# Performance work log

Measured on AMD Instinct MI355X. Metric: run time of the kernel, lower is better.

The kernel has to match this reference:

```python
import jax, jax.numpy as jnp
import numpy as np

B = 512      # batch = envs * nagents
M = 32       # nmodels
NAG = 8      # nagents
H = 256      # hidsz
NACT = 16    # nactions


def _lm(x, W, b, ids):
    # LinearMulti: per-example weight selected by model id.
    # x: [B, I], W: [M, I, O], b: [M, O], ids: [B] -> [B, O]
    return jnp.einsum('bi,bio->bo', x, W[ids]) + b[ids]


def setup_inputs() -> dict:
    key = jax.random.key(0)
    ks = jax.random.split(key, 16)
    s = 0.02
    return {
        'comm_in': jax.random.normal(ks[0], (B, NAG, H), jnp.float32),
        'inp': jnp.zeros((B, 1), jnp.int32),  # Embedding table has 1 row -> only index 0 valid
        'prev_hid': jax.random.normal(ks[1], (B, H), jnp.float32),
        'prev_cell': jnp.zeros((B, H), jnp.float32),  # unused in rnn branch, kept for signature fidelity
        'model_ids': jax.random.randint(ks[2], (B,), 0, M),
        # comm2hid LinearMulti (comm_encoder): hidsz -> hidsz
        'Wc': jax.random.normal(ks[3], (M, H, H), jnp.float32) * s,
        'bc': jax.random.normal(ks[4], (M, H), jnp.float32) * s,
        # rnn LinearMulti: hidsz -> hidsz
        'Wr': jax.random.normal(ks[5], (M, H, H), jnp.float32) * s,
        'br': jax.random.normal(ks[6], (M, H), jnp.float32) * s,
        # action LinearMulti: hidsz -> nactions
        'Wa': jax.random.normal(ks[7], (M, H, NACT), jnp.float32) * s,
        'ba': jax.random.normal(ks[8], (M, NACT), jnp.float32) * s,
        # baseline LinearMulti: hidsz -> 1
        'Wb': jax.random.normal(ks[9], (M, H, 1), jnp.float32) * s,
        'bb': jax.random.normal(ks[10], (M, 1), jnp.float32) * s,
        # comm_out LinearMulti (fully_connected): hidsz -> hidsz * nagents
        'Wo': jax.random.normal(ks[11], (M, H, H * NAG), jnp.float32) * s,
        'bo': jax.random.normal(ks[12], (M, H * NAG), jnp.float32) * s,
        # Encoder: Embedding(1, hidsz) + bias
        'lut': jax.random.normal(ks[13], (1, H), jnp.float32) * s,
        'enc_bias': jax.random.normal(ks[14], (H,), jnp.float32) * s,
    }


def reference(comm_in, inp, prev_hid, prev_cell, model_ids,
              Wc, bc, Wr, br, Wa, ba, Wb, bb, Wo, bo, lut, enc_bias):
    # __comm2hid: sum agent messages, then model-id-routed linear
    comm2hid = _lm(jnp.sum(comm_in, axis=1), Wc, bc, model_ids)  # [B, H]
    # Encoder: embedding lookup, sum over token dim, add bias
    enc = jnp.sum(lut[inp], axis=1) + enc_bias                   # [B, H]
    # _rnn: sum of encoder, routed recurrent linear, and comm; tanh gate
    hidstate = jnp.tanh(enc + _lm(prev_hid, Wr, br, model_ids) + comm2hid)
    # __action
    action_prob = jax.nn.softmax(_lm(hidstate, Wa, ba, model_ids), axis=-1)  # [B, NACT]
    baseline = _lm(hidstate, Wb, bb, model_ids)                              # [B, 1]
    # __comm_out (fully_connected): routed linear then divide by nagents-1
    comm_out = _lm(hidstate, Wo, bo, model_ids) / (NAG - 1)                  # [B, H*NAG]
    return (action_prob, baseline, hidstate, comm_out)
```

## Files before the change

kernel.cpp:

```cpp
#include <hip/hip_runtime.h>


constexpr int Bn = 512, Mn = 32, NAGn = 8, Hn = 256, NACTn = 16;
constexpr int On = Hn * NAGn;
constexpr int En = 32;
constexpr int EW = 8;

__device__ __forceinline__ void gl_lds16(const float* g, float* l) {
  __builtin_amdgcn_global_load_lds(
      (const __attribute__((address_space(1))) void*)g,
      (__attribute__((address_space(3))) void*)l, 16, 0, 0);
}


__global__ __launch_bounds__(512) void k_group(const int* __restrict__ ids,
                                               int* __restrict__ list32) {
  __shared__ int scnt[Mn];
  int t = threadIdx.x;
  if (t < Mn) scnt[t] = 0;
  list32[t] = -1;
  list32[t + 512] = -1;
  __syncthreads();
  int m = ids[t];
  int pos = atomicAdd(&scnt[m], 1);
  if (pos < En) list32[m * En + pos] = t;
}

__global__ __launch_bounds__(256) void k_pack(
    const float* __restrict__ comm_in, const float* __restrict__ prev_hid,
    const int* __restrict__ list32, float* __restrict__ xcat) {
  int m = blockIdx.x, half = blockIdx.y;
  int tid = threadIdx.x;
  __shared__ float buf[En][Hn + 1];
  __shared__ int lst[En];
  if (tid < En) lst[tid] = list32[m * En + tid];
  __syncthreads();
  if (half == 0) {
    for (int j = 0; j < En; j++) {
      int e = lst[j];
      float s = 0.f;
      if (e >= 0) {
        const float* cp = comm_in + (size_t)e * NAGn * Hn + tid;
#pragma unroll
        for (int a = 0; a < NAGn; a++) s += cp[a * Hn];
      }
      buf[j][tid] = s;
    }
  } else {
    for (int j = 0; j < En; j++) {
      int e = lst[j];
      buf[j][tid] = (e >= 0) ? prev_hid[e * Hn + tid] : 0.f;
    }
  }
  __syncthreads();
  int j = tid & 31, kr = tid >> 5;
  float* xm = xcat + ((size_t)m * 512 + half * Hn) * En;
  for (int k0 = 0; k0 < Hn; k0 += 8) {
    int k = k0 + kr;
    xm[(size_t)k * En + j] = buf[j][k];
  }
}

__global__ __launch_bounds__(256) void k_lin(
    const float* __restrict__ Wc, const float* __restrict__ Wr,
    const float* __restrict__ xcat, const int* __restrict__ list32,
    float* __restrict__ acc_hid) {
  int ct = blockIdx.x, kc = blockIdx.y, m = blockIdx.z;
  if (list32[m * En] < 0) return;
  int tid = threadIdx.x, w = tid >> 6, lane = tid & 63;
  __shared__ alignas(16) float xbuf[128 * En];
  __shared__ alignas(16) float wbuf[2][32 * 128];

  const float* W = (kc < 2) ? (Wc + ((size_t)m * Hn + kc * 128) * Hn)
                            : (Wr + ((size_t)m * Hn + (kc - 2) * 128) * Hn);
  const float* wsrc = W + ct * 128;
  const float* xsrc = xcat + ((size_t)m * 512 + kc * 128) * En;
#pragma unroll
  for (int q = 0; q < 4; q++) {
    int c = w * 4 + q;
    gl_lds16(xsrc + c * 256 + lane * 4, xbuf + c * 256);
  }
#pragma unroll
  for (int q = 0; q < 4; q++) {
    int c = w * 4 + q;
    int row = c * 2 + (lane >> 5);
    gl_lds16(wsrc + (size_t)row * Hn + (lane & 31) * 4, wbuf[0] + c * 256);
  }
  bool act = list32[m * En + w * EW] >= 0;
  float2 acc[EW];
#pragma unroll
  for (int j = 0; j < EW; j++) acc[j] = make_float2(0.f, 0.f);
  __syncthreads();

  for (int t = 0; t < 4; t++) {
    if (t < 3) {
      const float* ws2 = wsrc + (size_t)(t + 1) * 32 * Hn;
#pragma unroll
      for (int q = 0; q < 4; q++) {
        int c = w * 4 + q;
        int row = c * 2 + (lane >> 5);
        gl_lds16(ws2 + (size_t)row * Hn + (lane & 31) * 4, wbuf[(t + 1) & 1] + c * 256);
      }
    }
    if (act) {
      const float* wb = wbuf[t & 1] + lane * 2;
      const float* xb = xbuf + (size_t)(t * 32) * En + w * EW;
#pragma unroll 8
      for (int k = 0; k < 32; k++) {
        float2 wv = *(const float2*)(wb + k * 128);
        float4 xa = *(const float4*)(xb + k * En);
        float4 xc = *(const float4*)(xb + k * En + 4);
        acc[0].x += xa.x * wv.x; acc[0].y += xa.x * wv.y;
        acc[1].x += xa.y * wv.x; acc[1].y += xa.y * wv.y;
        acc[2].x += xa.z * wv.x; acc[2].y += xa.z * wv.y;
        acc[3].x += xa.w * wv.x; acc[3].y += xa.w * wv.y;
        acc[4].x += xc.x * wv.x; acc[4].y += xc.x * wv.y;
        acc[5].x += xc.y * wv.x; acc[5].y += xc.y * wv.y;
        acc[6].x += xc.z * wv.x; acc[6].y += xc.z * wv.y;
        acc[7].x += xc.w * wv.x; acc[7].y += xc.w * wv.y;
      }
    }
    __syncthreads();
  }
  if (act) {
    float* ap = acc_hid + ((size_t)m * En + w * EW) * Hn + ct * 128 + lane * 2;
#pragma unroll
    for (int j = 0; j < EW; j++) {
      atomicAdd(ap + (size_t)j * Hn,     acc[j].x);
      atomicAdd(ap + (size_t)j * Hn + 1, acc[j].y);
    }
  }
}

__global__ __launch_bounds__(256) void k_fin(
    const float* __restrict__ acc_hid, const float* __restrict__ bc,
    const float* __restrict__ br, const int* __restrict__ inp,
    const float* __restrict__ lut, const float* __restrict__ enc_bias,
    const int* __restrict__ list32, float* __restrict__ hid,
    float* __restrict__ xh) {
  int m = blockIdx.x, cs4 = blockIdx.y;
  int tid = threadIdx.x, lane = tid & 63, jw = tid >> 6;
  int col = cs4 * 64 + lane;
  __shared__ float hb[En][65];
  __shared__ int lst[En];
  if (tid < En) lst[tid] = list32[m * En + tid];
  __syncthreads();
  float bsum = bc[m * Hn + col] + br[m * Hn + col] + enc_bias[col];
  for (int jj = 0; jj < EW; jj++) {
    int j = jw * EW + jj;
    int e = lst[j];
    float h = 0.f;
    if (e >= 0) {
      float t = acc_hid[((size_t)m * En + j) * Hn + col] + bsum;
      int tok = inp[e];
      t += lut[(size_t)tok * Hn + col];
      h = tanhf(t);
      hid[(size_t)e * Hn + col] = h;
    }
    hb[j][lane] = h;
  }
  __syncthreads();
  int j2 = tid & 31, kr = tid >> 5;
  for (int k0 = 0; k0 < 64; k0 += 8) {
    int kl = k0 + kr;
    xh[((size_t)m * Hn + cs4 * 64 + kl) * En + j2] = hb[j2][kl];
  }
}

__global__ __launch_bounds__(256) void k_out(
    const float* __restrict__ Wo, const float* __restrict__ xh,
    const float* __restrict__ bo, const int* __restrict__ list32,
    float* __restrict__ comm_out) {
  int ct = blockIdx.x, m = blockIdx.y;
  if (list32[m * En] < 0) return;
  int tid = threadIdx.x, w = tid >> 6, lane = tid & 63;
  __shared__ alignas(16) float xbuf[Hn * En];
  __shared__ alignas(16) float wbuf[2][32 * 128];

  const float* xsrc = xh + (size_t)m * Hn * En;
#pragma unroll
  for (int q = 0; q < 8; q++) {
    int c = w * 8 + q;
    gl_lds16(xsrc + c * 256 + lane * 4, xbuf + c * 256);
  }
  const float* wsrc = Wo + (size_t)m * Hn * On + ct * 128;
#pragma unroll
  for (int q = 0; q < 4; q++) {
    int c = w * 4 + q;
    int row = c * 2 + (lane >> 5);
    gl_lds16(wsrc + (size_t)row * On + (lane & 31) * 4, wbuf[0] + c * 256);
  }
  bool act = list32[m * En + w * EW] >= 0;
  float2 acc[EW];
#pragma unroll
  for (int j = 0; j < EW; j++) acc[j] = make_float2(0.f, 0.f);
  __syncthreads();

  for (int t = 0; t < 8; t++) {
    if (t < 7) {
      const float* ws2 = wsrc + (size_t)(t + 1) * 32 * On;
#pragma unroll
      for (int q = 0; q < 4; q++) {
        int c = w * 4 + q;
        int row = c * 2 + (lane >> 5);
        gl_lds16(ws2 + (size_t)row * On + (lane & 31) * 4, wbuf[(t + 1) & 1] + c * 256);
      }
    }
    if (act) {
      const float* wb = wbuf[t & 1] + lane * 2;
      const float* xb = xbuf + (size_t)(t * 32) * En + w * EW;
#pragma unroll 8
      for (int k = 0; k < 32; k++) {
        float2 wv = *(const float2*)(wb + k * 128);
        float4 xa = *(const float4*)(xb + k * En);
        float4 xc = *(const float4*)(xb + k * En + 4);
        acc[0].x += xa.x * wv.x; acc[0].y += xa.x * wv.y;
        acc[1].x += xa.y * wv.x; acc[1].y += xa.y * wv.y;
        acc[2].x += xa.z * wv.x; acc[2].y += xa.z * wv.y;
        acc[3].x += xa.w * wv.x; acc[3].y += xa.w * wv.y;
        acc[4].x += xc.x * wv.x; acc[4].y += xc.x * wv.y;
        acc[5].x += xc.y * wv.x; acc[5].y += xc.y * wv.y;
        acc[6].x += xc.z * wv.x; acc[6].y += xc.z * wv.y;
        acc[7].x += xc.w * wv.x; acc[7].y += xc.w * wv.y;
      }
    }
    __syncthreads();
  }
  if (act) {
    float2 bv = *(const float2*)(bo + (size_t)m * On + ct * 128 + lane * 2);
    const float inv = 1.f / 7.f;
#pragma unroll
    for (int jj = 0; jj < EW; jj++) {
      int e = list32[m * En + w * EW + jj];
      if (e < 0) continue;
      float2 o;
      o.x = (acc[jj].x + bv.x) * inv;
      o.y = (acc[jj].y + bv.y) * inv;
      *(float2*)(comm_out + (size_t)e * On + ct * 128 + lane * 2) = o;
    }
  }
}

__global__ __launch_bounds__(64) void k_act(
    const float* __restrict__ hid, const float* __restrict__ Wa,
    const float* __restrict__ ba, const float* __restrict__ Wb,
    const float* __restrict__ bb, const int* __restrict__ ids,
    float* __restrict__ aprob, float* __restrict__ bl) {
  int b = blockIdx.x;
  int m = ids[b];
  int l = threadIdx.x;
  int o = l & 15;
  int kk = l >> 4;

  const float* wap = Wa + (size_t)m * Hn * NACTn + l;
  const float* hbase = hid + (size_t)b * Hn;
  float al = 0.f;
  for (int w16 = 0; w16 < 4; w16++) {
    float wv[16], hv[16];
#pragma unroll
    for (int il = 0; il < 16; il++) wv[il] = wap[(w16 * 16 + il) * 64];
#pragma unroll
    for (int il = 0; il < 16; il++) hv[il] = hbase[w16 * 64 + il * 4 + kk];
#pragma unroll
    for (int il = 0; il < 16; il++) al += wv[il] * hv[il];
  }
  al += __shfl_xor(al, 16);
  al += __shfl_xor(al, 32);
  al += ba[m * NACTn + o];

  float mx = al;
  mx = fmaxf(mx, __shfl_xor(mx, 1));
  mx = fmaxf(mx, __shfl_xor(mx, 2));
  mx = fmaxf(mx, __shfl_xor(mx, 4));
  mx = fmaxf(mx, __shfl_xor(mx, 8));
  float ex = expf(al - mx);
  float sm = ex;
  sm += __shfl_xor(sm, 1);
  sm += __shfl_xor(sm, 2);
  sm += __shfl_xor(sm, 4);
  sm += __shfl_xor(sm, 8);
  if (l < 16) aprob[b * NACTn + l] = ex / sm;

  float pb = 0.f;
  const float* wbp = Wb + (size_t)m * Hn;
  {
    float wv[4], hv[4];
#pragma unroll
    for (int k = 0; k < 4; k++) { wv[k] = wbp[l + k * 64]; hv[k] = hbase[l + k * 64]; }
#pragma unroll
    for (int k = 0; k < 4; k++) pb += wv[k] * hv[k];
  }
  pb += __shfl_xor(pb, 1);
  pb += __shfl_xor(pb, 2);
  pb += __shfl_xor(pb, 4);
  pb += __shfl_xor(pb, 8);
  pb += __shfl_xor(pb, 16);
  pb += __shfl_xor(pb, 32);
  if (l == 0) bl[b] = pb + bb[m];
}

extern "C" void kernel_launch(void* const* d_in, const int* in_sizes, int n_in,
                              void* d_out, int out_size, void* d_ws, size_t ws_size,
                              hipStream_t stream) {
  const float* comm_in  = (const float*)d_in[0];
  const int*   inp      = (const int*)d_in[1];
  const float* prev_hid = (const float*)d_in[2];
  const int*   ids      = (const int*)d_in[4];
  const float* Wc = (const float*)d_in[5];
  const float* bc = (const float*)d_in[6];
  const float* Wr = (const float*)d_in[7];
  const float* br = (const float*)d_in[8];
  const float* Wa = (const float*)d_in[9];
  const float* ba = (const float*)d_in[10];
  const float* Wb = (const float*)d_in[11];
  const float* bb = (const float*)d_in[12];
  const float* Wo = (const float*)d_in[13];
  const float* bo = (const float*)d_in[14];
  const float* lut      = (const float*)d_in[15];
  const float* enc_bias = (const float*)d_in[16];

  float* out      = (float*)d_out;
  float* aprob    = out;
  float* bl       = out + Bn * NACTn;
  float* hid      = out + Bn * NACTn + Bn;
  float* comm_out = hid + Bn * Hn;

  char* ws = (char*)d_ws;
  int*   list32  = (int*)ws;
  float* xcat    = (float*)(ws + 4096);
  float* xh      = xcat;
  float* acc_hid = (float*)(ws + 4096 + 2097152);

  k_group<<<1, 512, 0, stream>>>(ids, list32);
  hipMemsetAsync(acc_hid, 0, (size_t)Mn * En * Hn * 4, stream);
  k_pack<<<dim3(Mn, 2), 256, 0, stream>>>(comm_in, prev_hid, list32, xcat);
  k_lin<<<dim3(2, 4, Mn), 256, 0, stream>>>(Wc, Wr, xcat, list32, acc_hid);
  k_fin<<<dim3(Mn, 4), 256, 0, stream>>>(acc_hid, bc, br, inp, lut, enc_bias,
                                         list32, hid, xh);
  k_out<<<dim3(16, Mn), 256, 0, stream>>>(Wo, xh, bo, list32, comm_out);
  k_act<<<Bn, 64, 0, stream>>>(hid, Wa, ba, Wb, bb, ids, aprob, bl);
}
```

Baseline: 187.8 us.

## Fuse hidden linear with tanh finalize, drop split-K atomics and memset

```diff
diff --git a/kernel.cpp b/kernel.cpp
--- a/kernel.cpp
+++ b/kernel.cpp
@@ -61,30 +61,32 @@
   }
 }
 
-__global__ __launch_bounds__(256) void k_lin(
+__global__ __launch_bounds__(256) void k_linF(
     const float* __restrict__ Wc, const float* __restrict__ Wr,
-    const float* __restrict__ xcat, const int* __restrict__ list32,
-    float* __restrict__ acc_hid) {
-  int ct = blockIdx.x, kc = blockIdx.y, m = blockIdx.z;
+    const float* __restrict__ xcat, const float* __restrict__ bc,
+    const float* __restrict__ br, const int* __restrict__ inp,
+    const float* __restrict__ lut, const float* __restrict__ enc_bias,
+    const int* __restrict__ list32, float* __restrict__ hid,
+    float* __restrict__ xh) {
+  int ct = blockIdx.x, m = blockIdx.y;
   if (list32[m * En] < 0) return;
   int tid = threadIdx.x, w = tid >> 6, lane = tid & 63;
-  __shared__ alignas(16) float xbuf[128 * En];
+  __shared__ alignas(16) float xbuf[512 * En];
   __shared__ alignas(16) float wbuf[2][32 * 128];
 
-  const float* W = (kc < 2) ? (Wc + ((size_t)m * Hn + kc * 128) * Hn)
-                            : (Wr + ((size_t)m * Hn + (kc - 2) * 128) * Hn);
-  const float* wsrc = W + ct * 128;
-  const float* xsrc = xcat + ((size_t)m * 512 + kc * 128) * En;
-#pragma unroll
-  for (int q = 0; q < 4; q++) {
-    int c = w * 4 + q;
+  const float* xsrc = xcat + (size_t)m * 512 * En;
+#pragma unroll
+  for (int q = 0; q < 16; q++) {
+    int c = w * 16 + q;
     gl_lds16(xsrc + c * 256 + lane * 4, xbuf + c * 256);
   }
+  const float* wcs = Wc + (size_t)m * Hn * Hn + ct * 128;
+  const float* wrs = Wr + (size_t)m * Hn * Hn + ct * 128;
 #pragma unroll
   for (int q = 0; q < 4; q++) {
     int c = w * 4 + q;
     int row = c * 2 + (lane >> 5);
-    gl_lds16(wsrc + (size_t)row * Hn + (lane & 31) * 4, wbuf[0] + c * 256);
+    gl_lds16(wcs + (size_t)row * Hn + (lane & 31) * 4, wbuf[0] + c * 256);
   }
   bool act = list32[m * En + w * EW] >= 0;
   float2 acc[EW];
@@ -92,14 +94,16 @@
   for (int j = 0; j < EW; j++) acc[j] = make_float2(0.f, 0.f);
   __syncthreads();
 
-  for (int t = 0; t < 4; t++) {
-    if (t < 3) {
-      const float* ws2 = wsrc + (size_t)(t + 1) * 32 * Hn;
+  for (int t = 0; t < 16; t++) {
+    if (t < 15) {
+      int tn = t + 1;
+      const float* src = (tn < 8) ? (wcs + (size_t)tn * 32 * Hn)
+                                  : (wrs + (size_t)(tn - 8) * 32 * Hn);
 #pragma unroll
       for (int q = 0; q < 4; q++) {
         int c = w * 4 + q;
         int row = c * 2 + (lane >> 5);
-        gl_lds16(ws2 + (size_t)row * Hn + (lane & 31) * 4, wbuf[(t + 1) & 1] + c * 256);
+        gl_lds16(src + (size_t)row * Hn + (lane & 31) * 4, wbuf[tn & 1] + c * 256);
       }
     }
     if (act) {
@@ -122,48 +126,34 @@
     }
     __syncthreads();
   }
-  if (act) {
-    float* ap = acc_hid + ((size_t)m * En + w * EW) * Hn + ct * 128 + lane * 2;
-#pragma unroll
-    for (int j = 0; j < EW; j++) {
-      atomicAdd(ap + (size_t)j * Hn,     acc[j].x);
-      atomicAdd(ap + (size_t)j * Hn + 1, acc[j].y);
-    }
-  }
-}
-
-__global__ __launch_bounds__(256) void k_fin(
-    const float* __restrict__ acc_hid, const float* __restrict__ bc,
-    const float* __restrict__ br, const int* __restrict__ inp,
-    const float* __restrict__ lut, const float* __restrict__ enc_bias,
-    const int* __restrict__ list32, float* __restrict__ hid,
-    float* __restrict__ xh) {
-  int m = blockIdx.x, cs4 = blockIdx.y;
-  int tid = threadIdx.x, lane = tid & 63, jw = tid >> 6;
-  int col = cs4 * 64 + lane;
-  __shared__ float hb[En][65];
-  __shared__ int lst[En];
-  if (tid < En) lst[tid] = list32[m * En + tid];
-  __syncthreads();
-  float bsum = bc[m * Hn + col] + br[m * Hn + col] + enc_bias[col];
-  for (int jj = 0; jj < EW; jj++) {
-    int j = jw * EW + jj;
-    int e = lst[j];
-    float h = 0.f;
-    if (e >= 0) {
-      float t = acc_hid[((size_t)m * En + j) * Hn + col] + bsum;
-      int tok = inp[e];
-      t += lut[(size_t)tok * Hn + col];
-      h = tanhf(t);
-      hid[(size_t)e * Hn + col] = h;
-    }
-    hb[j][lane] = h;
-  }
-  __syncthreads();
-  int j2 = tid & 31, kr = tid >> 5;
-  for (int k0 = 0; k0 < 64; k0 += 8) {
-    int kl = k0 + kr;
-    xh[((size_t)m * Hn + cs4 * 64 + kl) * En + j2] = hb[j2][kl];
+
+  float* hb = (float*)wbuf;
+  int col = ct * 128 + lane * 2;
+  float2 bcv = *(const float2*)(bc + (size_t)m * Hn + col);
+  float2 brv = *(const float2*)(br + (size_t)m * Hn + col);
+  float2 ebv = *(const float2*)(enc_bias + col);
+#pragma unroll
+  for (int j = 0; j < EW; j++) {
+    int jj = w * EW + j;
+    float h0 = 0.f, h1 = 0.f;
+    if (act) {
+      int e = list32[m * En + jj];
+      if (e >= 0) {
+        int tok = inp[e];
+        float2 lv = *(const float2*)(lut + (size_t)tok * Hn + col);
+        h0 = tanhf(acc[j].x + bcv.x + brv.x + ebv.x + lv.x);
+        h1 = tanhf(acc[j].y + bcv.y + brv.y + ebv.y + lv.y);
+        *(float2*)(hid + (size_t)e * Hn + col) = make_float2(h0, h1);
+      }
+    }
+    hb[jj * 133 + lane * 2]     = h0;
+    hb[jj * 133 + lane * 2 + 1] = h1;
+  }
+  __syncthreads();
+  int j2 = tid & 31, r = tid >> 5;
+  for (int i = 0; i < 16; i++) {
+    int row = i * 8 + r;
+    xh[((size_t)m * Hn + ct * 128 + row) * En + j2] = hb[j2 * 133 + row];
   }
 }
 
@@ -326,17 +316,14 @@
   float* comm_out = hid + Bn * Hn;
 
   char* ws = (char*)d_ws;
-  int*   list32  = (int*)ws;
-  float* xcat    = (float*)(ws + 4096);
-  float* xh      = xcat;
-  float* acc_hid = (float*)(ws + 4096 + 2097152);
+  int*   list32 = (int*)ws;
+  float* xcat   = (float*)(ws + 4096);
+  float* xh     = (float*)(ws + 4096 + 2097152);
 
   k_group<<<1, 512, 0, stream>>>(ids, list32);
-  hipMemsetAsync(acc_hid, 0, (size_t)Mn * En * Hn * 4, stream);
   k_pack<<<dim3(Mn, 2), 256, 0, stream>>>(comm_in, prev_hid, list32, xcat);
-  k_lin<<<dim3(2, 4, Mn), 256, 0, stream>>>(Wc, Wr, xcat, list32, acc_hid);
-  k_fin<<<dim3(Mn, 4), 256, 0, stream>>>(acc_hid, bc, br, inp, lut, enc_bias,
-                                         list32, hid, xh);
+  k_linF<<<dim3(2, Mn), 256, 0, stream>>>(Wc, Wr, xcat, bc, br, inp, lut,
+                                          enc_bias, list32, hid, xh);
   k_out<<<dim3(16, Mn), 256, 0, stream>>>(Wo, xh, bo, list32, comm_out);
   k_act<<<Bn, 64, 0, stream>>>(hid, Wa, ba, Wb, bb, ids, aprob, bl);
 }
```

Result: slower. 202.4 us (+7.8%).
